# Kernel tuning notes

Hardware: AMD Instinct MI355X
Metric: run time of the kernel (lower is better)

Reference implementation:

```python
import jax, jax.numpy as jnp
import numpy as np

D_MODEL = 1024
H = 16
D_HEAD = D_MODEL // H  # 64
RANK = 32
ALPHA = 1.0


def _lora_linear(x, W, b, dW, dB):
    # merged weight: W + alpha * (dB @ dW), then x @ W_merged.T + b
    Wm = W + ALPHA * (dB @ dW)
    return x @ Wm.T + b


def setup_inputs() -> dict:
    key = jax.random.key(0)
    ks = jax.random.split(key, 20)
    inp = {"x": jax.random.normal(ks[0], (2, 2048, D_MODEL), dtype=jnp.float32)}
    i = 1
    for name in ("q", "k", "v", "o"):
        inp[f"{name}_W"] = jax.random.normal(ks[i], (D_MODEL, D_MODEL), dtype=jnp.float32) * 0.02; i += 1
        inp[f"{name}_b"] = jnp.zeros((D_MODEL,), dtype=jnp.float32)
        inp[f"{name}_dW"] = jax.random.normal(ks[i], (RANK, D_MODEL), dtype=jnp.float32) * 0.01; i += 1
        inp[f"{name}_dB"] = jax.random.normal(ks[i], (D_MODEL, RANK), dtype=jnp.float32) * 0.01; i += 1
    return inp


def reference(x, q_W, q_b, q_dW, q_dB, k_W, k_b, k_dW, k_dB,
              v_W, v_b, v_dW, v_dB, o_W, o_b, o_dW, o_dB):
    b_s, n, _ = x.shape
    # LoRA-merged QKV projections
    q = _lora_linear(x, q_W, q_b, q_dW, q_dB).reshape(b_s, n, H, D_HEAD)
    k = _lora_linear(x, k_W, k_b, k_dW, k_dB).reshape(b_s, n, H, D_HEAD)
    v = _lora_linear(x, v_W, v_b, v_dW, v_dB).reshape(b_s, n, H, D_HEAD)
    scale = 1.0 / np.sqrt(D_HEAD).astype(np.float32)
    # att: [b, h, nq, nk]
    att = jnp.einsum('bqhd,bkhd->bhqk', q, k) * scale
    att = jax.nn.softmax(att, axis=-1)  # dropout = identity (eval mode)
    out = jnp.einsum('bhqk,bkhd->bqhd', att, v).reshape(b_s, n, H * D_HEAD)
    return _lora_linear(out, o_W, o_b, o_dW, o_dB)
```

## Files before the change

kernel.cpp:

```cpp
#include <hip/hip_runtime.h>

typedef unsigned short ushort_t;
typedef unsigned int u32;
typedef __attribute__((ext_vector_type(8))) short short8;
typedef __attribute__((ext_vector_type(4))) float floatx4;

typedef const __attribute__((address_space(1))) u32* gptr_t;
typedef __attribute__((address_space(3))) u32* lptr_t;

__device__ __forceinline__ void async_copy16(void* lds, const void* g) {
  __builtin_amdgcn_global_load_lds((gptr_t)g, (lptr_t)lds, 16, 0, 0);
}

__device__ __forceinline__ ushort_t f2bf(float f) {
  u32 u = __float_as_uint(f);
  u += 0x7fffu + ((u >> 16) & 1u);
  return (ushort_t)(u >> 16);
}

__device__ __forceinline__ floatx4 mfma16(short8 a, short8 b, floatx4 c) {
  return __builtin_amdgcn_mfma_f32_16x16x32_bf16(a, b, c, 0, 0, 0);
}

struct alignas(16) F4 { float a, b, c, d; };
struct alignas(8) U4 { ushort_t a, b, c, d; };

#define QSCALE 0.18033688011112043f

__global__ __launch_bounds__(256) void prep_kernel(
    const float* __restrict__ x, ushort_t* __restrict__ xs,
    const float* __restrict__ W0, const float* __restrict__ dW0, const float* __restrict__ dB0,
    const float* __restrict__ W1, const float* __restrict__ dW1, const float* __restrict__ dB1,
    const float* __restrict__ W2, const float* __restrict__ dW2, const float* __restrict__ dB2,
    const float* __restrict__ W3, const float* __restrict__ dW3, const float* __restrict__ dB3,
    ushort_t* __restrict__ Wm) {
  const int bid = blockIdx.x;
  if (bid < 4096) {
    int i = bid * 256 + threadIdx.x;
    F4 v = ((const F4*)x)[i];
    U4 hh = {f2bf(v.a), f2bf(v.b), f2bf(v.c), f2bf(v.d)};
    ((U4*)xs)[i] = hh;
    return;
  }
  const int t = bid - 4096;
  const int layer = t >> 7, sub = t & 127;
  const float* W = (layer == 0) ? W0 : (layer == 1) ? W1 : (layer == 2) ? W2 : W3;
  const float* dW = (layer == 0) ? dW0 : (layer == 1) ? dW1 : (layer == 2) ? dW2 : dW3;
  const float* dB = (layer == 0) ? dB0 : (layer == 1) ? dB1 : (layer == 2) ? dB2 : dB3;
  ushort_t* Wh = Wm + (size_t)layer * 1024 * 1024;
  const int ot = sub * 8;
  const int d0 = threadIdx.x * 4;
  float acc[8][4] = {};
  for (int r = 0; r < 32; ++r) {
    F4 w = *(const F4*)&dW[r * 1024 + d0];
    float wv[4] = {w.a, w.b, w.c, w.d};
#pragma unroll
    for (int o = 0; o < 8; ++o) {
      float s = dB[(ot + o) * 32 + r];
#pragma unroll
      for (int j = 0; j < 4; ++j) acc[o][j] += s * wv[j];
    }
  }
#pragma unroll
  for (int o = 0; o < 8; ++o) {
    F4 w = *(const F4*)&W[(ot + o) * 1024 + d0];
    U4 hh = {f2bf(w.a + acc[o][0]), f2bf(w.b + acc[o][1]),
             f2bf(w.c + acc[o][2]), f2bf(w.d + acc[o][3])};
    *(U4*)&Wh[(ot + o) * 1024 + d0] = hh;
  }
}

template <int MODE, int TN>
__global__ __launch_bounds__(256) void gemm_bt(
    const ushort_t* __restrict__ A, const ushort_t* __restrict__ B,
    const float* __restrict__ b0, const float* __restrict__ b1,
    const float* __restrict__ b2,
    ushort_t* __restrict__ C, ushort_t* __restrict__ vth,
    float* __restrict__ Cf, const int M, const int N, const int K) {
  constexpr int NT2 = TN / 32;
  __shared__ __align__(16) ushort_t lA[2][128 * 32], lB[2][TN * 32];
  const int tid = threadIdx.x;
  const int wave = tid >> 6, lane = tid & 63;
  const int lo4 = lane & 15, quad = lane >> 4;
  const int n0 = blockIdx.x * TN, m0 = blockIdx.y * 128;
  const int wm = (wave >> 1) * 64, wn = (wave & 1) * (TN / 2);

  floatx4 acc[4][NT2];
  const floatx4 zero4 = {0.f, 0.f, 0.f, 0.f};
#pragma unroll
  for (int mt = 0; mt < 4; ++mt)
#pragma unroll
    for (int nt = 0; nt < NT2; ++nt) acc[mt][nt] = zero4;

  const int strow = lane >> 2;
  const int stcol = (lane & 3) * 8;

  const int NTILES = K >> 5;
  {
#pragma unroll
    for (int i = 0; i < 2; ++i) {
      const int g = wave * 2 + i;
      async_copy16(&lA[0][g * 512], A + (size_t)(m0 + g * 16 + strow) * K + stcol);
    }
#pragma unroll
    for (int i = 0; i < TN / 64; ++i) {
      const int g = wave * (TN / 64) + i;
      async_copy16(&lB[0][g * 512], B + (size_t)(n0 + g * 16 + strow) * K + stcol);
    }
  }
  __syncthreads();

  for (int t = 0; t < NTILES; ++t) {
    const int cur = t & 1;
    if (t + 1 < NTILES) {
      const int kk = (t + 1) << 5;
#pragma unroll
      for (int i = 0; i < 2; ++i) {
        const int g = wave * 2 + i;
        async_copy16(&lA[cur ^ 1][g * 512], A + (size_t)(m0 + g * 16 + strow) * K + kk + stcol);
      }
#pragma unroll
      for (int i = 0; i < TN / 64; ++i) {
        const int g = wave * (TN / 64) + i;
        async_copy16(&lB[cur ^ 1][g * 512], B + (size_t)(n0 + g * 16 + strow) * K + kk + stcol);
      }
    }
    short8 a_[4], b_[NT2];
#pragma unroll
    for (int t2 = 0; t2 < 4; ++t2)
      a_[t2] = *(const short8*)&lA[cur][(wm + t2 * 16 + lo4) * 32 + quad * 8];
#pragma unroll
    for (int t2 = 0; t2 < NT2; ++t2)
      b_[t2] = *(const short8*)&lB[cur][(wn + t2 * 16 + lo4) * 32 + quad * 8];
#pragma unroll
    for (int mt = 0; mt < 4; ++mt)
#pragma unroll
      for (int nt = 0; nt < NT2; ++nt) acc[mt][nt] = mfma16(a_[mt], b_[nt], acc[mt][nt]);
    if (t + 1 < NTILES) __syncthreads();
  }

#pragma unroll
  for (int nt = 0; nt < NT2; ++nt) {
    const int col = n0 + wn + nt * 16 + lo4;
    float bias;
    if (MODE == 0)
      bias = (col < 1024) ? b0[col] : (col < 2048) ? b1[col - 1024] : b2[col - 2048];
    else
      bias = b0[col];
#pragma unroll
    for (int mt = 0; mt < 4; ++mt)
#pragma unroll
      for (int r = 0; r < 4; ++r) {
        const int row = m0 + wm + mt * 16 + quad * 4 + r;
        float c = acc[mt][nt][r] + bias;
        if (MODE == 0) {
          if (col < 1024) c *= QSCALE;
          ushort_t hv = f2bf(c);
          if (col < 2048) {
            C[(size_t)row * 2048 + col] = hv;
          } else {
            const int d = col - 2048;
            const size_t vrow = (size_t)(((row >> 11) * 16 + (d >> 6)) * 64 + (d & 63));
            vth[vrow * 2048 + (row & 2047)] = hv;
          }
        } else {
          Cf[(size_t)row * N + col] = c;
        }
      }
  }
}

__global__ __launch_bounds__(512) void attn_kernel(
    const ushort_t* __restrict__ qk, const ushort_t* __restrict__ vt,
    ushort_t* __restrict__ at) {
  __shared__ __align__(16) ushort_t Kh[2][64 * 64], Vh[2][64 * 64];
  __shared__ __align__(16) ushort_t P[8][16][72];
  const int qt = blockIdx.x, bh = blockIdx.y;
  const int b = bh >> 4, h = bh & 15;
  const int tid = threadIdx.x;
  const int wave = tid >> 6, lane = tid & 63;
  const int lo4 = lane & 15, quad = lane >> 4;

  short8 qh[2];
  {
    const size_t g = (size_t)(b * 2048 + qt * 128 + wave * 16 + lo4) * 2048 + h * 64 + quad * 8;
    qh[0] = *(const short8*)(qk + g);
    qh[1] = *(const short8*)(qk + g + 32);
  }
  float l_acc[4] = {0.f, 0.f, 0.f, 0.f};
  const floatx4 zero4 = {0.f, 0.f, 0.f, 0.f};
  floatx4 O[4];
#pragma unroll
  for (int nt = 0; nt < 4; ++nt) O[nt] = zero4;

  const int strow = lane >> 3;
  const int stcol = ((lane & 7) ^ strow) * 8;
  const int srow = wave * 8 + strow;
  const int uoff = wave * 8 * 64;

  async_copy16(&Kh[0][uoff], qk + (size_t)(b * 2048 + srow) * 2048 + 1024 + h * 64 + stcol);
  async_copy16(&Vh[0][uoff], vt + (size_t)(bh * 64 + srow) * 2048 + stcol);
  __syncthreads();

  for (int kt = 0; kt < 32; ++kt) {
    const int cur = kt & 1;
    if (kt + 1 < 32) {
      const int kn = (kt + 1) * 64;
      async_copy16(&Kh[cur ^ 1][uoff],
                   qk + (size_t)(b * 2048 + kn + srow) * 2048 + 1024 + h * 64 + stcol);
      async_copy16(&Vh[cur ^ 1][uoff], vt + (size_t)(bh * 64 + srow) * 2048 + kn + stcol);
    }

    floatx4 s[4];
#pragma unroll
    for (int nt = 0; nt < 4; ++nt) s[nt] = zero4;
#pragma unroll
    for (int nt = 0; nt < 4; ++nt)
#pragma unroll
      for (int ks = 0; ks < 2; ++ks) {
        const int off = (nt * 16 + lo4) * 64 + (((ks * 4 + quad) ^ (lo4 & 7)) * 8);
        s[nt] = mfma16(qh[ks], *(const short8*)&Kh[cur][off], s[nt]);
      }

#pragma unroll
    for (int nt = 0; nt < 4; ++nt)
#pragma unroll
      for (int r = 0; r < 4; ++r) {
        float pv = __builtin_amdgcn_exp2f(s[nt][r]);
        s[nt][r] = pv;
        P[wave][quad * 4 + r][nt * 16 + lo4] = (ushort_t)(__float_as_uint(pv) >> 16);
      }
#pragma unroll
    for (int r = 0; r < 4; ++r)
      l_acc[r] += (s[0][r] + s[1][r]) + (s[2][r] + s[3][r]);

#pragma unroll
    for (int ks = 0; ks < 2; ++ks) {
      short8 pf = *(const short8*)&P[wave][lo4][ks * 32 + quad * 8];
#pragma unroll
      for (int nt = 0; nt < 4; ++nt) {
        const int off = (nt * 16 + lo4) * 64 + (((ks * 4 + quad) ^ (lo4 & 7)) * 8);
        O[nt] = mfma16(pf, *(const short8*)&Vh[cur][off], O[nt]);
      }
    }
    if (kt + 1 < 32) __syncthreads();
  }

  float linv[4];
#pragma unroll
  for (int r = 0; r < 4; ++r) {
    float s = l_acc[r];
    s += __shfl_xor(s, 1);
    s += __shfl_xor(s, 2);
    s += __shfl_xor(s, 4);
    s += __shfl_xor(s, 8);
    linv[r] = 1.f / s;
  }
#pragma unroll
  for (int nt = 0; nt < 4; ++nt)
#pragma unroll
    for (int r = 0; r < 4; ++r) {
      float o = O[nt][r] * linv[r];
      const size_t row = (size_t)(b * 2048 + qt * 128 + wave * 16 + quad * 4 + r);
      at[row * 1024 + h * 64 + nt * 16 + lo4] = f2bf(o);
    }
}

extern "C" void kernel_launch(void* const* d_in, const int* in_sizes, int n_in,
                              void* d_out, int out_size, void* d_ws, size_t ws_size,
                              hipStream_t stream) {
  const float* x = (const float*)d_in[0];
  const float* qW = (const float*)d_in[1];
  const float* qb = (const float*)d_in[2];
  const float* qdW = (const float*)d_in[3];
  const float* qdB = (const float*)d_in[4];
  const float* kW = (const float*)d_in[5];
  const float* kb = (const float*)d_in[6];
  const float* kdW = (const float*)d_in[7];
  const float* kdB = (const float*)d_in[8];
  const float* vW = (const float*)d_in[9];
  const float* vb = (const float*)d_in[10];
  const float* vdW = (const float*)d_in[11];
  const float* vdB = (const float*)d_in[12];
  const float* oW = (const float*)d_in[13];
  const float* ob = (const float*)d_in[14];
  const float* odW = (const float*)d_in[15];
  const float* odB = (const float*)d_in[16];

  char* ws = (char*)d_ws;
  const size_t MB = 1024u * 1024u;
  const size_t WELEM = 1024u * 1024u;
  ushort_t* xs = (ushort_t*)(ws + 0 * MB);
  ushort_t* Wm = (ushort_t*)(ws + 8 * MB);
  ushort_t* qk = (ushort_t*)(ws + 16 * MB);
  ushort_t* vt = (ushort_t*)(ws + 32 * MB);
  ushort_t* at = xs;

  prep_kernel<<<4608, 256, 0, stream>>>(x, xs, qW, qdW, qdB, kW, kdW, kdB,
                                        vW, vdW, vdB, oW, odW, odB, Wm);
  gemm_bt<0, 128><<<dim3(24, 32), 256, 0, stream>>>(xs, Wm, qb, kb, vb,
                                                    qk, vt, nullptr, 4096, 3072, 1024);
  attn_kernel<<<dim3(16, 32), 512, 0, stream>>>(qk, vt, at);
  gemm_bt<1, 64><<<dim3(16, 32), 256, 0, stream>>>(at, Wm + 3 * WELEM, ob, nullptr,
                                                   nullptr, nullptr, nullptr,
                                                   (float*)d_out, 4096, 1024, 1024);
}
```

Measured before the change: 236.6 us.

## Rework attention to 32x32 MFMA with register-resident P via permlane swaps

The attention kernel moves from 16x16x32 to 32x32x16 bf16 MFMA, with each of 4 waves handling 32 query rows instead of 8 waves with 16. It computes S transposed, so the exp'd probabilities can be packed with v_cvt_pk_bf16 and rearranged in registers with permlane32_swap, removing the LDS round-trip for P. It also adds s_setprio around MFMA blocks and halves the threads per block. The intent is fewer LDS accesses and better MFMA efficiency, at the cost of more registers per wave and fewer waves to hide latency.

```diff
diff --git a/kernel.cpp b/kernel.cpp
--- a/kernel.cpp
+++ b/kernel.cpp
@@ -4,6 +4,9 @@
 typedef unsigned int u32;
 typedef __attribute__((ext_vector_type(8))) short short8;
 typedef __attribute__((ext_vector_type(4))) float floatx4;
+typedef __attribute__((ext_vector_type(16))) float floatx16;
+typedef __attribute__((ext_vector_type(2))) unsigned int uintx2;
+typedef __attribute__((ext_vector_type(4))) unsigned int uintx4;
 
 typedef const __attribute__((address_space(1))) u32* gptr_t;
 typedef __attribute__((address_space(3))) u32* lptr_t;
@@ -20,6 +23,24 @@
 
 __device__ __forceinline__ floatx4 mfma16(short8 a, short8 b, floatx4 c) {
   return __builtin_amdgcn_mfma_f32_16x16x32_bf16(a, b, c, 0, 0, 0);
+}
+
+__device__ __forceinline__ floatx16 mfma32(short8 a, short8 b, floatx16 c) {
+  return __builtin_amdgcn_mfma_f32_32x32x16_bf16(a, b, c, 0, 0, 0);
+}
+
+__device__ __forceinline__ u32 cvt_pk_bf16(float lo, float hi) {
+  u32 r;
+  asm("v_cvt_pk_bf16_f32 %0, %1, %2" : "=v"(r) : "v"(lo), "v"(hi));
+  return r;
+}
+
+__device__ __forceinline__ short8 mkfrag(u32 x0, u32 x1, u32 x2, u32 x3) {
+  uintx2 ra = __builtin_amdgcn_permlane32_swap(x0, x2, false, false);
+  uintx2 rb = __builtin_amdgcn_permlane32_swap(x1, x3, false, false);
+  union { uintx4 u; short8 s; } t;
+  t.u[0] = ra[0]; t.u[1] = rb[0]; t.u[2] = ra[1]; t.u[3] = rb[1];
+  return t.s;
 }
 
 struct alignas(16) F4 { float a, b, c, d; };
@@ -170,99 +191,107 @@
   }
 }
 
-__global__ __launch_bounds__(512) void attn_kernel(
+__global__ __launch_bounds__(256) void attn_kernel(
     const ushort_t* __restrict__ qk, const ushort_t* __restrict__ vt,
     ushort_t* __restrict__ at) {
-  __shared__ __align__(16) ushort_t Kh[2][64 * 64], Vh[2][64 * 64];
-  __shared__ __align__(16) ushort_t P[8][16][72];
+  __shared__ __align__(16) ushort_t Kh[2][64 * 64];
+  __shared__ __align__(16) ushort_t Vh[2][64 * 64];
   const int qt = blockIdx.x, bh = blockIdx.y;
   const int b = bh >> 4, h = bh & 15;
   const int tid = threadIdx.x;
   const int wave = tid >> 6, lane = tid & 63;
-  const int lo4 = lane & 15, quad = lane >> 4;
-
-  short8 qh[2];
+  const int l31 = lane & 31, hi = lane >> 5, l7 = lane & 7;
+
+  short8 qf[4];
   {
-    const size_t g = (size_t)(b * 2048 + qt * 128 + wave * 16 + lo4) * 2048 + h * 64 + quad * 8;
-    qh[0] = *(const short8*)(qk + g);
-    qh[1] = *(const short8*)(qk + g + 32);
-  }
+    const ushort_t* g =
+        qk + (size_t)(b * 2048 + qt * 128 + wave * 32 + l31) * 2048 + h * 64 + hi * 8;
+#pragma unroll
+    for (int st = 0; st < 4; ++st) qf[st] = *(const short8*)(g + st * 16);
+  }
+
+  floatx16 O[2];
+#pragma unroll
+  for (int i = 0; i < 16; ++i) { O[0][i] = 0.f; O[1][i] = 0.f; }
   float l_acc[4] = {0.f, 0.f, 0.f, 0.f};
-  const floatx4 zero4 = {0.f, 0.f, 0.f, 0.f};
-  floatx4 O[4];
-#pragma unroll
-  for (int nt = 0; nt < 4; ++nt) O[nt] = zero4;
 
   const int strow = lane >> 3;
-  const int stcol = ((lane & 7) ^ strow) * 8;
-  const int srow = wave * 8 + strow;
-  const int uoff = wave * 8 * 64;
-
-  async_copy16(&Kh[0][uoff], qk + (size_t)(b * 2048 + srow) * 2048 + 1024 + h * 64 + stcol);
-  async_copy16(&Vh[0][uoff], vt + (size_t)(bh * 64 + srow) * 2048 + stcol);
+  const int stswz = (l7 ^ strow) * 8;
+  const int r0 = wave * 16 + strow, r1 = r0 + 8;
+  const int u0 = wave * 1024, u1 = u0 + 512;
+  const ushort_t* Ksrc = qk + (size_t)b * 2048 * 2048 + 1024 + h * 64;
+  const ushort_t* Vsrc = vt + (size_t)bh * 64 * 2048;
+
+#define STAGE(buf, kt_)                                                  \
+  {                                                                      \
+    const int kn = (kt_)*64;                                             \
+    async_copy16(&Kh[buf][u0], Ksrc + (size_t)(kn + r0) * 2048 + stswz); \
+    async_copy16(&Kh[buf][u1], Ksrc + (size_t)(kn + r1) * 2048 + stswz); \
+    async_copy16(&Vh[buf][u0], Vsrc + (size_t)r0 * 2048 + kn + stswz);   \
+    async_copy16(&Vh[buf][u1], Vsrc + (size_t)r1 * 2048 + kn + stswz);   \
+  }
+
+  STAGE(0, 0);
   __syncthreads();
 
   for (int kt = 0; kt < 32; ++kt) {
     const int cur = kt & 1;
-    if (kt + 1 < 32) {
-      const int kn = (kt + 1) * 64;
-      async_copy16(&Kh[cur ^ 1][uoff],
-                   qk + (size_t)(b * 2048 + kn + srow) * 2048 + 1024 + h * 64 + stcol);
-      async_copy16(&Vh[cur ^ 1][uoff], vt + (size_t)(bh * 64 + srow) * 2048 + kn + stcol);
-    }
-
-    floatx4 s[4];
-#pragma unroll
-    for (int nt = 0; nt < 4; ++nt) s[nt] = zero4;
-#pragma unroll
-    for (int nt = 0; nt < 4; ++nt)
-#pragma unroll
-      for (int ks = 0; ks < 2; ++ks) {
-        const int off = (nt * 16 + lo4) * 64 + (((ks * 4 + quad) ^ (lo4 & 7)) * 8);
-        s[nt] = mfma16(qh[ks], *(const short8*)&Kh[cur][off], s[nt]);
-      }
-
-#pragma unroll
-    for (int nt = 0; nt < 4; ++nt)
-#pragma unroll
-      for (int r = 0; r < 4; ++r) {
-        float pv = __builtin_amdgcn_exp2f(s[nt][r]);
-        s[nt][r] = pv;
-        P[wave][quad * 4 + r][nt * 16 + lo4] = (ushort_t)(__float_as_uint(pv) >> 16);
-      }
-#pragma unroll
-    for (int r = 0; r < 4; ++r)
-      l_acc[r] += (s[0][r] + s[1][r]) + (s[2][r] + s[3][r]);
-
-#pragma unroll
-    for (int ks = 0; ks < 2; ++ks) {
-      short8 pf = *(const short8*)&P[wave][lo4][ks * 32 + quad * 8];
-#pragma unroll
-      for (int nt = 0; nt < 4; ++nt) {
-        const int off = (nt * 16 + lo4) * 64 + (((ks * 4 + quad) ^ (lo4 & 7)) * 8);
-        O[nt] = mfma16(pf, *(const short8*)&Vh[cur][off], O[nt]);
-      }
-    }
+    if (kt + 1 < 32) STAGE(cur ^ 1, kt + 1);
+
+    floatx16 s0, s1;
+#pragma unroll
+    for (int i = 0; i < 16; ++i) { s0[i] = 0.f; s1[i] = 0.f; }
+    __builtin_amdgcn_s_setprio(1);
+#pragma unroll
+    for (int st = 0; st < 4; ++st) {
+      const int c = ((st * 2 + hi) ^ l7) * 8;
+      s0 = mfma32(*(const short8*)&Kh[cur][l31 * 64 + c], qf[st], s0);
+      s1 = mfma32(*(const short8*)&Kh[cur][(32 + l31) * 64 + c], qf[st], s1);
+    }
+    __builtin_amdgcn_s_setprio(0);
+
+    u32 a0[8], a1[8];
+#pragma unroll
+    for (int j = 0; j < 8; ++j) {
+      float p0a = __builtin_amdgcn_exp2f(s0[2 * j]);
+      float p0b = __builtin_amdgcn_exp2f(s0[2 * j + 1]);
+      float p1a = __builtin_amdgcn_exp2f(s1[2 * j]);
+      float p1b = __builtin_amdgcn_exp2f(s1[2 * j + 1]);
+      l_acc[j & 3] += (p0a + p0b) + (p1a + p1b);
+      a0[j] = cvt_pk_bf16(p0a, p0b);
+      a1[j] = cvt_pk_bf16(p1a, p1b);
+    }
+
+    short8 pb00 = mkfrag(a0[0], a0[1], a0[2], a0[3]);
+    short8 pb01 = mkfrag(a0[4], a0[5], a0[6], a0[7]);
+    short8 pb10 = mkfrag(a1[0], a1[1], a1[2], a1[3]);
+    short8 pb11 = mkfrag(a1[4], a1[5], a1[6], a1[7]);
+
+    __builtin_amdgcn_s_setprio(1);
+#pragma unroll
+    for (int dblk = 0; dblk < 2; ++dblk) {
+      const int vr = (dblk * 32 + l31) * 64;
+      O[dblk] = mfma32(*(const short8*)&Vh[cur][vr + ((0 + hi) ^ l7) * 8], pb00, O[dblk]);
+      O[dblk] = mfma32(*(const short8*)&Vh[cur][vr + ((2 + hi) ^ l7) * 8], pb01, O[dblk]);
+      O[dblk] = mfma32(*(const short8*)&Vh[cur][vr + ((4 + hi) ^ l7) * 8], pb10, O[dblk]);
+      O[dblk] = mfma32(*(const short8*)&Vh[cur][vr + ((6 + hi) ^ l7) * 8], pb11, O[dblk]);
+    }
+    __builtin_amdgcn_s_setprio(0);
     if (kt + 1 < 32) __syncthreads();
   }
-
-  float linv[4];
-#pragma unroll
-  for (int r = 0; r < 4; ++r) {
-    float s = l_acc[r];
-    s += __shfl_xor(s, 1);
-    s += __shfl_xor(s, 2);
-    s += __shfl_xor(s, 4);
-    s += __shfl_xor(s, 8);
-    linv[r] = 1.f / s;
-  }
-#pragma unroll
-  for (int nt = 0; nt < 4; ++nt)
-#pragma unroll
-    for (int r = 0; r < 4; ++r) {
-      float o = O[nt][r] * linv[r];
-      const size_t row = (size_t)(b * 2048 + qt * 128 + wave * 16 + quad * 4 + r);
-      at[row * 1024 + h * 64 + nt * 16 + lo4] = f2bf(o);
+#undef STAGE
+
+  float l = (l_acc[0] + l_acc[1]) + (l_acc[2] + l_acc[3]);
+  l += __shfl_xor(l, 32);
+  const float linv = 1.f / l;
+  ushort_t* out = at + (size_t)(b * 2048 + qt * 128 + wave * 32 + l31) * 1024 + h * 64;
+#pragma unroll
+  for (int dblk = 0; dblk < 2; ++dblk)
+#pragma unroll
+    for (int g = 0; g < 4; ++g) {
+      U4 hh = {f2bf(O[dblk][4 * g + 0] * linv), f2bf(O[dblk][4 * g + 1] * linv),
+               f2bf(O[dblk][4 * g + 2] * linv), f2bf(O[dblk][4 * g + 3] * linv)};
+      *(U4*)&out[dblk * 32 + g * 8 + hi * 4] = hh;
     }
 }
 
@@ -300,7 +329,7 @@
                                         vW, vdW, vdB, oW, odW, odB, Wm);
   gemm_bt<0, 128><<<dim3(24, 32), 256, 0, stream>>>(xs, Wm, qb, kb, vb,
                                                     qk, vt, nullptr, 4096, 3072, 1024);
-  attn_kernel<<<dim3(16, 32), 512, 0, stream>>>(qk, vt, at);
+  attn_kernel<<<dim3(16, 32), 256, 0, stream>>>(qk, vt, at);
   gemm_bt<1, 64><<<dim3(16, 32), 256, 0, stream>>>(at, Wm + 3 * WELEM, ob, nullptr,
                                                    nullptr, nullptr, nullptr,
                                                    (float*)d_out, 4096, 1024, 1024);
```

New measurement: 227.1 us. 4.0% less time.
